# Kernel tuning notes

Hardware: AMD Instinct MI355X
Metric: run time of the kernel (lower is better)

## Reference

```python
import jax, jax.numpy as jnp
import numpy as np
from jax import lax

# Static config (matches init_kwargs)
D_MODEL = 1024
EXPAND = 2
D_INNER = D_MODEL * EXPAND          # 2048
HEAD_DIM = 64
N_HEADS = D_INNER // HEAD_DIM       # 32
N_GROUPS = 1
D_STATE = 128
D_CONV = 4
CONV_DIM = D_INNER + 2 * N_GROUPS * D_STATE        # 2304
D_IN_PROJ = 2 * D_INNER + 2 * N_GROUPS * D_STATE + N_HEADS  # 4384
SEQLEN = 8192
LN_EPS = 1e-5


def setup_inputs() -> dict:
    key = jax.random.key(0)
    ks = jax.random.split(key, 6)
    x = jax.random.normal(ks[0], (SEQLEN, D_MODEL), jnp.float32)
    W_in = jax.random.normal(ks[1], (D_IN_PROJ, D_MODEL), jnp.float32) / np.sqrt(D_MODEL)
    W_conv = jax.random.normal(ks[2], (CONV_DIM, 1, D_CONV), jnp.float32) / np.sqrt(D_CONV)
    b_conv = jnp.zeros((CONV_DIM,), jnp.float32)
    # dt_bias init per Mamba2: dt ~ LogUniform(dt_min, dt_max), inverse-softplus
    dt = jnp.exp(jax.random.uniform(ks[3], (N_HEADS,)) * (np.log(0.1) - np.log(0.001)) + np.log(0.001))
    dt = jnp.clip(dt, 1e-4)
    dt_bias = dt + jnp.log(-jnp.expm1(-dt))
    A_log = jnp.log(jax.random.uniform(ks[4], (N_HEADS,), minval=1.0, maxval=16.0))
    D_param = jnp.ones((N_HEADS,), jnp.float32)
    ln_w = jnp.ones((D_INNER,), jnp.float32)
    ln_b = jnp.zeros((D_INNER,), jnp.float32)
    W_out = jax.random.normal(ks[5], (D_MODEL, D_INNER), jnp.float32) / np.sqrt(D_INNER)
    return dict(x=x, W_in=W_in, W_conv=W_conv, b_conv=b_conv, dt_bias=dt_bias,
                A_log=A_log, D_param=D_param, ln_w=ln_w, ln_b=ln_b, W_out=W_out)


def reference(x, W_in, W_conv, b_conv, dt_bias, A_log, D_param, ln_w, ln_b, W_out):
    L = x.shape[0]
    zxbcdt = x @ W_in.T                                   # (L, d_in_proj)
    z = zxbcdt[:, :D_INNER]                               # gate
    xbc = zxbcdt[:, D_INNER:D_INNER + CONV_DIM]           # (L, conv_dim)
    dt = jax.nn.softplus(zxbcdt[:, D_INNER + CONV_DIM:] + dt_bias)  # (L, h)
    # depthwise causal-window conv with SAME padding over the sequence
    lhs = xbc.T[None]                                      # (1, conv_dim, L)
    conv = lax.conv_general_dilated(lhs, W_conv, (1,), 'SAME',
                                    feature_group_count=CONV_DIM,
                                    dimension_numbers=('NCH', 'OIH', 'NCH'))[0]
    xbc = jax.nn.silu((conv + b_conv[:, None]).T)          # (L, conv_dim)
    x_ssm = xbc[:, :D_INNER].reshape(L, N_HEADS, HEAD_DIM)
    B = xbc[:, D_INNER:D_INNER + N_GROUPS * D_STATE].reshape(L, N_GROUPS, D_STATE)
    C = xbc[:, D_INNER + N_GROUPS * D_STATE:].reshape(L, N_GROUPS, D_STATE)
    hpg = N_HEADS // N_GROUPS
    Bh = jnp.repeat(B, hpg, axis=1)                        # (L, h, n)
    Ch = jnp.repeat(C, hpg, axis=1)                        # (L, h, n)
    A = -jnp.exp(A_log)                                    # (h,), negative
    a = jnp.exp(dt * A)                                    # (L, h) per-token decay in (0,1)
    V = x_ssm * dt[..., None]                              # discretized input (L, h, p)
    # non-causal SSD (VSSD): global state H then readout, plus D skip
    H = jnp.einsum('lhn,lh,lhp->hnp', Bh, a, V)            # (h, n, p)
    y = jnp.einsum('lhn,hnp->lhp', Ch, H) + D_param[None, :, None] * x_ssm
    y = y.reshape(L, D_INNER)
    # LayerNorm (eqx default: weight+bias, eps=1e-5), then gate by z
    mu = jnp.mean(y, axis=-1, keepdims=True)
    var = jnp.var(y, axis=-1, keepdims=True)
    y = ((y - mu) / jnp.sqrt(var + LN_EPS)) * ln_w + ln_b
    y = y * z
    return y @ W_out.T                                     # (L, d_model)
```

## Files before the change

kernel.cpp:

```cpp
#include <hip/hip_runtime.h>
#include <hip/hip_bf16.h>
#include <math.h>

#define L_SEQ 8192
#define DM 1024
#define DI 2048
#define NH 32
#define HD 64
#define DS 128
#define CDIM 2304
#define DPROJ 4384
#define NPAD_IN 4608
#define KSPLIT 16
#define OPROWS 2176

typedef short bf16x8 __attribute__((ext_vector_type(8)));
typedef float floatx4 __attribute__((ext_vector_type(4)));
typedef unsigned short u16x4 __attribute__((ext_vector_type(4)));
typedef unsigned short u16x8 __attribute__((ext_vector_type(8)));

#define AS1(p) ((const __attribute__((address_space(1))) void*)(p))
#define AS3(p) ((__attribute__((address_space(3))) void*)(p))

__device__ __forceinline__ float bf2f(unsigned short u) {
  union { unsigned int i; float f; } c; c.i = ((unsigned int)u) << 16; return c.f;
}
__device__ __forceinline__ unsigned short f2bf(float f) {
  return __bfloat16_as_ushort(__float2bfloat16(f));
}

template <int OMODE>
__global__ __launch_bounds__(512, 6)
void gemm128_tlp3(const unsigned short* __restrict__ A, int lda,
                  const unsigned short* __restrict__ B, int ldb,
                  void* __restrict__ Cout, int ldc,
                  int K, int Nstore) {
  __shared__ __align__(16) char lds[49152];
  const int t = threadIdx.x;
  const int lane = t & 63;
  const int w = t >> 6;
  const int wm = w & 1, wn = w >> 1;
  const int fr = lane & 15, quad = lane >> 4;

  int gx = gridDim.x, gy = gridDim.y;
  int linear = blockIdx.y * gx + blockIdx.x;
  int xcd = linear & 7, loc = linear >> 3;
  int mper = gy >> 3;
  int mt = xcd * mper + loc % mper;
  int nt = loc / mper;
  const int m0 = mt << 7, n0 = nt << 7;
  const int NT = K >> 5;

  floatx4 acc[4][2];
#pragma unroll
  for (int i = 0; i < 4; ++i)
#pragma unroll
    for (int j = 0; j < 2; ++j) acc[i][j] = (floatx4){0.f, 0.f, 0.f, 0.f};
  bf16x8 af[4], bb[2];

  auto stA = [&](int slot, int kt) {
    int o = t * 16;
    int os = o ^ (((o >> 7) & 7) << 4);
    int r128 = os >> 7, half = (os >> 6) & 1, kb = os & 63;
    int R = (half << 6) | r128;
    const unsigned short* src = A + (size_t)(m0 + R) * lda + (kt << 5) + (kb >> 1);
    __builtin_amdgcn_global_load_lds(AS1(src), AS3(lds + slot * 16384 + o), 16, 0, 0);
  };
  auto stB = [&](int slot, int kt) {
    int o = t * 16;
    int os = o ^ (((o >> 7) & 7) << 4);
    int r128 = os >> 7, half = (os >> 6) & 1, kb = os & 63;
    int R = (half << 6) | r128;
    const unsigned short* src = B + (size_t)(n0 + R) * ldb + (kt << 5) + (kb >> 1);
    __builtin_amdgcn_global_load_lds(AS1(src), AS3(lds + slot * 16384 + 8192 + o), 16, 0, 0);
  };
  auto rdA = [&](int slot, int mi) -> bf16x8 {
    int r128 = (mi << 4) | fr;
    int chunk = ((wm << 2) | quad) ^ (fr & 7);
    return *(const bf16x8*)(lds + slot * 16384 + r128 * 128 + chunk * 16);
  };
  auto rdB = [&](int slot, int ni) -> bf16x8 {
    int R = (wn << 5) | (ni << 4) | fr;
    int r128 = R & 63, half = R >> 6;
    int chunk = ((half << 2) | quad) ^ (fr & 7);
    return *(const bf16x8*)(lds + slot * 16384 + 8192 + r128 * 128 + chunk * 16);
  };

  stA(0, 0); stB(0, 0);
  if (NT > 1) {
    stA(1, 1); stB(1, 1);
    asm volatile("s_waitcnt vmcnt(2)" ::: "memory");
  } else {
    asm volatile("s_waitcnt vmcnt(0)" ::: "memory");
  }
  __builtin_amdgcn_s_barrier();

  int cur = 0;
  for (int kt = 0; kt < NT; ++kt) {
    const bool pf = (kt + 2 < NT);
#pragma unroll
    for (int mi = 0; mi < 4; ++mi) af[mi] = rdA(cur, mi);
    bb[0] = rdB(cur, 0); bb[1] = rdB(cur, 1);
    if (pf) {
      int s2 = cur + 2; if (s2 >= 3) s2 -= 3;
      stA(s2, kt + 2); stB(s2, kt + 2);
    }
    asm volatile("s_waitcnt lgkmcnt(0)" ::: "memory");
    __builtin_amdgcn_s_setprio(1);
#pragma unroll
    for (int mi = 0; mi < 4; ++mi) {
      acc[mi][0] = __builtin_amdgcn_mfma_f32_16x16x32_bf16(af[mi], bb[0], acc[mi][0], 0, 0, 0);
      acc[mi][1] = __builtin_amdgcn_mfma_f32_16x16x32_bf16(af[mi], bb[1], acc[mi][1], 0, 0, 0);
    }
    __builtin_amdgcn_s_setprio(0);
    if (kt < NT - 1) {
      if (pf) asm volatile("s_waitcnt vmcnt(2)" ::: "memory");
      else    asm volatile("s_waitcnt vmcnt(0)" ::: "memory");
      __builtin_amdgcn_s_barrier();
    }
    ++cur; if (cur == 3) cur = 0;
  }

  if (OMODE == 0) {
    __syncthreads();
    unsigned short* rp = (unsigned short*)lds;
    unsigned short* C = (unsigned short*)Cout;
    const int mb = wm * 64, nb = wn * 32;
#pragma unroll
    for (int mi = 0; mi < 4; ++mi)
#pragma unroll
      for (int ni = 0; ni < 2; ++ni)
#pragma unroll
        for (int r = 0; r < 4; ++r)
          rp[(mb + mi * 16 + quad * 4 + r) * 128 + nb + ni * 16 + fr] = f2bf(acc[mi][ni][r]);
    __syncthreads();
#pragma unroll
    for (int j = 0; j < 4; ++j) {
      int lin = j * 4096 + t * 8;
      int row = lin >> 7, col = lin & 127;
      int gcol = n0 + col;
      if (gcol < Nstore)
        *(u16x8*)&C[(size_t)(m0 + row) * ldc + gcol] = *(const u16x8*)&rp[lin];
    }
  } else {
    float* Cf = (float*)Cout;
#pragma unroll
    for (int mi = 0; mi < 4; ++mi)
#pragma unroll
      for (int ni = 0; ni < 2; ++ni) {
        int gcol = n0 + wn * 32 + ni * 16 + fr;
        int grow = m0 + wm * 64 + mi * 16 + quad * 4;
#pragma unroll
        for (int r = 0; r < 4; ++r)
          if (gcol < Nstore)
            Cf[(size_t)(grow + r) * ldc + gcol] = acc[mi][ni][r];
      }
  }
}

template <int MODE>
__global__ __launch_bounds__(256)
void gemm_bt_mfma(const unsigned short* __restrict__ A, int lda,
                  const unsigned short* __restrict__ B, int ldb,
                  void* __restrict__ Cout, int ldc,
                  int Kfull, int Nstore,
                  const unsigned short* __restrict__ xs,
                  const float* __restrict__ Dvec) {
  __shared__ __align__(16) char smem[17408];
  unsigned short* Asm = (unsigned short*)smem;
  unsigned short* Bsm = Asm + 128 * 32;
  const int t = threadIdx.x;

  int bx = blockIdx.x, by = blockIdx.y;
  if (MODE != 2) {
    int gx = gridDim.x;
    int linear = by * gx + bx;
    int xcd = linear & 7;
    int local = linear >> 3;
    by = xcd * 8 + (local & 7);
    bx = local >> 3;
  }
  const int m0 = by * 128;
  const int n0 = bx * 128;

  int kstart = 0, klen = Kfull;
  if (MODE == 2) { klen = Kfull / KSPLIT; kstart = blockIdx.z * klen; }
  const int wave = t >> 6, lane = t & 63;
  const int wm = (wave & 1) * 64;
  const int wn = (wave >> 1) * 64;
  const int fr = lane & 15;
  const int quad = lane >> 4;

  floatx4 acc[4][4];
#pragma unroll
  for (int i = 0; i < 4; ++i)
#pragma unroll
    for (int j = 0; j < 4; ++j) acc[i][j] = (floatx4){0.f, 0.f, 0.f, 0.f};

  for (int k0 = kstart; k0 < kstart + klen; k0 += 32) {
#pragma unroll
    for (int i = 0; i < 2; ++i) {
      int linear = i * 256 + t;
      int row = linear >> 2;
      int kq = (linear & 3) * 8;
      const unsigned short* ga = A + (size_t)(m0 + row) * lda + (k0 + kq);
      const unsigned short* gb = B + (size_t)(n0 + row) * ldb + (k0 + kq);
      __builtin_amdgcn_global_load_lds(AS1(ga), AS3(&Asm[linear * 8]), 16, 0, 0);
      __builtin_amdgcn_global_load_lds(AS1(gb), AS3(&Bsm[linear * 8]), 16, 0, 0);
    }
    __syncthreads();

    bf16x8 af[4], bfr[4];
#pragma unroll
    for (int i = 0; i < 4; ++i) {
      af[i]  = *(const bf16x8*)&Asm[(wm + i * 16 + fr) * 32 + quad * 8];
      bfr[i] = *(const bf16x8*)&Bsm[(wn + i * 16 + fr) * 32 + quad * 8];
    }
#pragma unroll
    for (int mi = 0; mi < 4; ++mi)
#pragma unroll
      for (int ni = 0; ni < 4; ++ni)
        acc[mi][ni] = __builtin_amdgcn_mfma_f32_16x16x32_bf16(
            af[mi], bfr[ni], acc[mi][ni], 0, 0, 0);
    __syncthreads();
  }

  const int lrbase = (wm ? 16 : 0) + quad * 4;
  if (MODE == 0 || MODE == 1) {
    unsigned short(*rp)[136] = (unsigned short(*)[136])smem;
    unsigned short* C = (unsigned short*)Cout;
#pragma unroll
    for (int mi = 0; mi < 4; ++mi) {
      __syncthreads();
#pragma unroll
      for (int ni = 0; ni < 4; ++ni)
#pragma unroll
        for (int r = 0; r < 4; ++r)
          rp[lrbase + r][wn + ni * 16 + fr] = f2bf(acc[mi][ni][r]);
      __syncthreads();
#pragma unroll
      for (int j = 0; j < 2; ++j) {
        int off = j * 2048 + t * 8;
        int lr = off >> 7, c = off & 127;
        int grow = m0 + (lr >> 4) * 64 + mi * 16 + (lr & 15);
        int gcol = n0 + c;
        u16x8 v = *(const u16x8*)&rp[lr][c];
        if (MODE == 1) {
          u16x8 xv = *(const u16x8*)&xs[(size_t)grow * ldc + gcol];
          float Dh = Dvec[gcol >> 6];
          u16x8 o;
#pragma unroll
          for (int e = 0; e < 8; ++e) o[e] = f2bf(bf2f(v[e]) + Dh * bf2f(xv[e]));
          *(u16x8*)&C[(size_t)grow * ldc + gcol] = o;
        } else {
          if (gcol < Nstore) *(u16x8*)&C[(size_t)grow * ldc + gcol] = v;
        }
      }
    }
  } else {
    float(*rpf)[136] = (float(*)[136])smem;
    float* C = (float*)Cout;
    if (MODE == 2) C += (size_t)blockIdx.z * DS * DI;
#pragma unroll
    for (int mi = 0; mi < 4; ++mi) {
      __syncthreads();
#pragma unroll
      for (int ni = 0; ni < 4; ++ni)
#pragma unroll
        for (int r = 0; r < 4; ++r)
          rpf[lrbase + r][wn + ni * 16 + fr] = acc[mi][ni][r];
      __syncthreads();
#pragma unroll
      for (int j = 0; j < 4; ++j) {
        int off = j * 1024 + t * 4;
        int lr = off >> 7, c = off & 127;
        int grow = m0 + (lr >> 4) * 64 + mi * 16 + (lr & 15);
        int gcol = n0 + c;
        float4 v = *(const float4*)&rpf[lr][c];
        *(float4*)&C[(size_t)grow * ldc + gcol] = v;
      }
    }
  }
}

__global__ __launch_bounds__(256)
void cast_all_kernel(const float* __restrict__ x, const float* __restrict__ W_in,
                     const float* __restrict__ W_out,
                     unsigned short* __restrict__ x_bf16,
                     unsigned short* __restrict__ win_bf16,
                     unsigned short* __restrict__ wout_bf16) {
  int b = blockIdx.x;
  int t = threadIdx.x;
  u16x4 o = (u16x4){0, 0, 0, 0};
  if (b < 8192) {
    size_t i4 = ((size_t)b * 256 + t) * 4;
    float4 v = *(const float4*)(x + i4);
    o.x = f2bf(v.x); o.y = f2bf(v.y); o.z = f2bf(v.z); o.w = f2bf(v.w);
    *(u16x4*)(x_bf16 + i4) = o;
  } else if (b < 12800) {
    size_t i4 = ((size_t)(b - 8192) * 256 + t) * 4;
    int row = (int)(i4 >> 10);
    if (row < DPROJ) {
      float4 v = *(const float4*)(W_in + i4);
      o.x = f2bf(v.x); o.y = f2bf(v.y); o.z = f2bf(v.z); o.w = f2bf(v.w);
    }
    *(u16x4*)(win_bf16 + i4) = o;
  } else {
    size_t i4 = ((size_t)(b - 12800) * 256 + t) * 4;
    float4 v = *(const float4*)(W_out + i4);
    o.x = f2bf(v.x); o.y = f2bf(v.y); o.z = f2bf(v.z); o.w = f2bf(v.w);
    *(u16x4*)(wout_bf16 + i4) = o;
  }
}

__global__ __launch_bounds__(256)
void dt_kernel(const unsigned short* __restrict__ zxb, const float* __restrict__ dt_bias,
               const float* __restrict__ A_log, float* __restrict__ s_out) {
  int idx = blockIdx.x * 256 + threadIdx.x;
  int l = idx >> 5, h = idx & 31;
  float v = bf2f(zxb[(size_t)l * DPROJ + (DI + CDIM) + h]) + dt_bias[h];
  float d = (v > 20.f) ? v : log1pf(expf(v));
  s_out[idx] = d * expf(-d * expf(A_log[h]));
}

__global__ __launch_bounds__(256)
void conv_fused_kernel(const unsigned short* __restrict__ zxb,
                       const float* __restrict__ Wc,
                       const float* __restrict__ bc,
                       const float* __restrict__ svec,
                       unsigned short* __restrict__ xs,
                       unsigned short* __restrict__ cb,
                       unsigned short* __restrict__ OpT) {
  __shared__ unsigned short zt[67][66];
  __shared__ unsigned short ot[64][66];
  __shared__ float sl[64];
  const int c0 = blockIdx.x * 64;
  const int l0 = blockIdx.y * 64;
  const int t = threadIdx.x;
  for (int idx = t; idx < 67 * 16; idx += 256) {
    int row = idx >> 4;
    int colq = (idx & 15) * 4;
    int gl = l0 - 1 + row;
    u16x4 v = (u16x4){0, 0, 0, 0};
    if (gl >= 0 && gl < L_SEQ)
      v = *(const u16x4*)&zxb[(size_t)gl * DPROJ + DI + c0 + colq];
    *(u16x4*)&zt[row][colq] = v;
  }
  const bool isX = (c0 < DI);
  const bool isC = (c0 >= DI + DS);
  if (isX && t < 64) sl[t] = svec[(size_t)(l0 + t) * NH + (c0 >> 6)];
  const int c = t & 63;
  const int gc = c0 + c;
  const float4 wv = *(const float4*)&Wc[gc * 4];
  const float bias = bc[gc];
  const int lq = (t >> 6) * 16;
  __syncthreads();
#pragma unroll
  for (int i = 0; i < 16; ++i) {
    int ll = lq + i;
    float sacc = bias + bf2f(zt[ll][c]) * wv.x + bf2f(zt[ll + 1][c]) * wv.y +
                 bf2f(zt[ll + 2][c]) * wv.z + bf2f(zt[ll + 3][c]) * wv.w;
    float v = sacc / (1.f + expf(-sacc));
    int gl = l0 + ll;
    if (isC) {
      cb[(size_t)gl * DS + (gc - (DI + DS))] = f2bf(v);
    } else if (isX) {
      xs[(size_t)gl * DI + gc] = f2bf(v);
      ot[c][ll] = f2bf(v * sl[ll]);
    } else {
      ot[c][ll] = f2bf(v);
    }
  }
  if (!isC) {
    __syncthreads();
#pragma unroll
    for (int j = 0; j < 4; ++j) {
      int linear = j * 1024 + t * 4;
      int rr = linear >> 6;
      int lc = linear & 63;
      *(u16x4*)&OpT[(size_t)(c0 + rr) * L_SEQ + l0 + lc] = *(const u16x4*)&ot[rr][lc];
    }
  }
}

__global__ __launch_bounds__(256)
void h_reduce_t_kernel(const float* __restrict__ P, unsigned short* __restrict__ Ht) {
  __shared__ float tile[32][65];
  const int bid = blockIdx.x;
  const int pt = bid & 31, ng = bid >> 5;
  const int t = threadIdx.x;
#pragma unroll
  for (int i = 0; i < 8; ++i) {
    int nl = i * 4 + (t >> 6);
    int n = ng * 32 + nl;
    int p = pt * 64 + (t & 63);
    float acc = 0.f;
#pragma unroll
    for (int z = 0; z < KSPLIT; ++z)
      acc += P[(size_t)z * (DS * DI) + (size_t)n * DI + p];
    tile[nl][t & 63] = acc;
  }
  __syncthreads();
#pragma unroll
  for (int j = 0; j < 8; ++j) {
    int linear = j * 256 + t;
    int pl = linear >> 5, nl = linear & 31;
    Ht[(size_t)(pt * 64 + pl) * DS + ng * 32 + nl] = f2bf(tile[nl][pl]);
  }
}

__global__ __launch_bounds__(256)
void ln_mul_kernel(const unsigned short* __restrict__ ybuf, unsigned short* __restrict__ zxb,
                   const float* __restrict__ ln_w, const float* __restrict__ ln_b) {
  int l = blockIdx.x;
  int t = threadIdx.x;
  int c0 = t * 8;
  u16x8 yv = *(const u16x8*)&ybuf[(size_t)l * DI + c0];
  float vals[8];
  float s = 0.f, sq = 0.f;
#pragma unroll
  for (int i = 0; i < 8; ++i) {
    float v = bf2f(yv[i]);
    vals[i] = v;
    s += v;
    sq += v * v;
  }
#pragma unroll
  for (int off = 32; off > 0; off >>= 1) {
    s += __shfl_down(s, off, 64);
    sq += __shfl_down(sq, off, 64);
  }
  __shared__ float red[10];
  int wave = t >> 6, lane = t & 63;
  if (lane == 0) { red[wave] = s; red[4 + wave] = sq; }
  __syncthreads();
  if (t == 0) {
    float S = red[0] + red[1] + red[2] + red[3];
    float SQ = red[4] + red[5] + red[6] + red[7];
    float mu = S / (float)DI;
    red[8] = mu;
    red[9] = rsqrtf(SQ / (float)DI - mu * mu + 1e-5f);
  }
  __syncthreads();
  float mu = red[8], rstd = red[9];
  unsigned short* zrow = zxb + (size_t)l * DPROJ;
  u16x8 zv = *(const u16x8*)&zrow[c0];
  float4 w0 = *(const float4*)&ln_w[c0], w1 = *(const float4*)&ln_w[c0 + 4];
  float4 b0 = *(const float4*)&ln_b[c0], b1 = *(const float4*)&ln_b[c0 + 4];
  float w[8] = {w0.x, w0.y, w0.z, w0.w, w1.x, w1.y, w1.z, w1.w};
  float b[8] = {b0.x, b0.y, b0.z, b0.w, b1.x, b1.y, b1.z, b1.w};
  u16x8 o;
#pragma unroll
  for (int i = 0; i < 8; ++i) {
    float v = (vals[i] - mu) * rstd * w[i] + b[i];
    o[i] = f2bf(v * bf2f(zv[i]));
  }
  *(u16x8*)&zrow[DI + c0] = o;
}

extern "C" void kernel_launch(void* const* d_in, const int* in_sizes, int n_in,
                              void* d_out, int out_size, void* d_ws, size_t ws_size,
                              hipStream_t stream) {
  const float* x       = (const float*)d_in[0];
  const float* W_in    = (const float*)d_in[1];
  const float* W_conv  = (const float*)d_in[2];
  const float* b_conv  = (const float*)d_in[3];
  const float* dt_bias = (const float*)d_in[4];
  const float* A_log   = (const float*)d_in[5];
  const float* D_param = (const float*)d_in[6];
  const float* ln_w    = (const float*)d_in[7];
  const float* ln_b    = (const float*)d_in[8];
  const float* W_out   = (const float*)d_in[9];
  float* out = (float*)d_out;

  unsigned short* zxb = (unsigned short*)d_ws;
  unsigned short* xs   = zxb + (size_t)L_SEQ * DPROJ;
  unsigned short* cb   = xs + (size_t)L_SEQ * DI;
  float* svec = (float*)(cb + (size_t)L_SEQ * DS);
  unsigned short* OpT = (unsigned short*)(svec + (size_t)L_SEQ * NH);
  float* Ppart = (float*)(OpT + (size_t)OPROWS * L_SEQ);
  unsigned short* Ht = (unsigned short*)(Ppart + (size_t)KSPLIT * DS * DI);
  unsigned short* wout_bf16 = Ht + (size_t)DI * DS;
  unsigned short* x_bf16   = OpT;
  unsigned short* win_bf16 = OpT + (size_t)L_SEQ * DM;
  unsigned short* ybuf     = OpT;

  cast_all_kernel<<<14848, 256, 0, stream>>>(x, W_in, W_out, x_bf16, win_bf16,
                                             wout_bf16);

  gemm128_tlp3<0><<<dim3(NPAD_IN / 128, L_SEQ / 128), 512, 0, stream>>>(
      x_bf16, DM, win_bf16, DM, zxb, DPROJ, DM, DPROJ);

  dt_kernel<<<(L_SEQ * NH) / 256, 256, 0, stream>>>(zxb, dt_bias, A_log, svec);

  conv_fused_kernel<<<dim3(CDIM / 64, L_SEQ / 64), 256, 0, stream>>>(
      zxb, W_conv, b_conv, svec, xs, cb, OpT);

  gemm_bt_mfma<2><<<dim3(DI / 128, 1, KSPLIT), 256, 0, stream>>>(
      OpT + (size_t)DI * L_SEQ, L_SEQ, OpT, L_SEQ, Ppart, DI, L_SEQ, DI,
      nullptr, nullptr);

  h_reduce_t_kernel<<<128, 256, 0, stream>>>(Ppart, Ht);

  gemm_bt_mfma<1><<<dim3(DI / 128, L_SEQ / 128), 256, 0, stream>>>(
      cb, DS, Ht, DS, ybuf, DI, DS, DI, xs, D_param);

  ln_mul_kernel<<<L_SEQ, 256, 0, stream>>>(ybuf, zxb, ln_w, ln_b);

  gemm128_tlp3<1><<<dim3(DM / 128, L_SEQ / 128), 512, 0, stream>>>(
      zxb + DI, DPROJ, wout_bf16, DI, out, DM, DI, DM);
}
```

Baseline: 340.1 us.

## Enlarge GEMM block tile to 256x128 with 4x2 warp layout

Changes the bf16 MFMA GEMM used for the input and output projections from a 128x128 to a 256x128 block tile. Each warp now computes a 64x64 sub-tile with 16 accumulators, and the B fragments are reloaded in two halves. The aim is more MFMA work per LDS load and less global traffic per output, at the cost of more LDS (72KB), more registers, lower occupancy (launch bound 4) and half as many blocks. The epilogue LDS staging now writes 256 rows x 128 bf16, which is 64KB and still fits in the 72KB buffer.

New measurement: 328.9 us. -3.3%, faster.

```diff
diff --git a/kernel.cpp b/kernel.cpp
--- a/kernel.cpp
+++ b/kernel.cpp
@@ -30,16 +30,16 @@
 }
 
 template <int OMODE>
-__global__ __launch_bounds__(512, 6)
-void gemm128_tlp3(const unsigned short* __restrict__ A, int lda,
-                  const unsigned short* __restrict__ B, int ldb,
-                  void* __restrict__ Cout, int ldc,
-                  int K, int Nstore) {
-  __shared__ __align__(16) char lds[49152];
+__global__ __launch_bounds__(512, 4)
+void gemm_v4(const unsigned short* __restrict__ A, int lda,
+             const unsigned short* __restrict__ B, int ldb,
+             void* __restrict__ Cout, int ldc,
+             int K, int Nstore) {
+  __shared__ __align__(16) char lds[73728];
   const int t = threadIdx.x;
   const int lane = t & 63;
   const int w = t >> 6;
-  const int wm = w & 1, wn = w >> 1;
+  const int wm = w & 3, wn = w >> 2;
   const int fr = lane & 15, quad = lane >> 4;
 
   int gx = gridDim.x, gy = gridDim.y;
@@ -48,48 +48,56 @@
   int mper = gy >> 3;
   int mt = xcd * mper + loc % mper;
   int nt = loc / mper;
-  const int m0 = mt << 7, n0 = nt << 7;
+  const int m0 = mt << 8, n0 = nt << 7;
   const int NT = K >> 5;
 
-  floatx4 acc[4][2];
+  floatx4 acc[4][4];
 #pragma unroll
   for (int i = 0; i < 4; ++i)
 #pragma unroll
-    for (int j = 0; j < 2; ++j) acc[i][j] = (floatx4){0.f, 0.f, 0.f, 0.f};
+    for (int j = 0; j < 4; ++j) acc[i][j] = (floatx4){0.f, 0.f, 0.f, 0.f};
   bf16x8 af[4], bb[2];
 
   auto stA = [&](int slot, int kt) {
-    int o = t * 16;
-    int os = o ^ (((o >> 7) & 7) << 4);
-    int r128 = os >> 7, half = (os >> 6) & 1, kb = os & 63;
-    int R = (half << 6) | r128;
-    const unsigned short* src = A + (size_t)(m0 + R) * lda + (kt << 5) + (kb >> 1);
-    __builtin_amdgcn_global_load_lds(AS1(src), AS3(lds + slot * 16384 + o), 16, 0, 0);
+#pragma unroll
+    for (int i = 0; i < 2; ++i) {
+      int o = i * 8192 + t * 16;
+      int os = o ^ (((o >> 7) & 7) << 4);
+      int r128 = os >> 7;
+      int half = (os >> 6) & 1;
+      int kb = os & 63;
+      int R = (half << 7) | r128;
+      const unsigned short* src = A + (size_t)(m0 + R) * lda + (kt << 5) + (kb >> 1);
+      __builtin_amdgcn_global_load_lds(AS1(src), AS3(lds + slot * 24576 + o), 16, 0, 0);
+    }
   };
   auto stB = [&](int slot, int kt) {
     int o = t * 16;
     int os = o ^ (((o >> 7) & 7) << 4);
-    int r128 = os >> 7, half = (os >> 6) & 1, kb = os & 63;
-    int R = (half << 6) | r128;
+    int r64 = os >> 7;
+    int half = (os >> 6) & 1;
+    int kb = os & 63;
+    int R = (half << 6) | r64;
     const unsigned short* src = B + (size_t)(n0 + R) * ldb + (kt << 5) + (kb >> 1);
-    __builtin_amdgcn_global_load_lds(AS1(src), AS3(lds + slot * 16384 + 8192 + o), 16, 0, 0);
+    __builtin_amdgcn_global_load_lds(AS1(src), AS3(lds + slot * 24576 + 16384 + o), 16, 0, 0);
   };
   auto rdA = [&](int slot, int mi) -> bf16x8 {
-    int r128 = (mi << 4) | fr;
-    int chunk = ((wm << 2) | quad) ^ (fr & 7);
-    return *(const bf16x8*)(lds + slot * 16384 + r128 * 128 + chunk * 16);
+    int R = (wm << 6) | (mi << 4) | fr;
+    int r128 = R & 127, half = R >> 7;
+    int chunk = ((half << 2) | quad) ^ (fr & 7);
+    return *(const bf16x8*)(lds + slot * 24576 + r128 * 128 + chunk * 16);
   };
   auto rdB = [&](int slot, int ni) -> bf16x8 {
-    int R = (wn << 5) | (ni << 4) | fr;
-    int r128 = R & 63, half = R >> 6;
+    int R = (wn << 6) | (ni << 4) | fr;
+    int r64 = R & 63, half = R >> 6;
     int chunk = ((half << 2) | quad) ^ (fr & 7);
-    return *(const bf16x8*)(lds + slot * 16384 + 8192 + r128 * 128 + chunk * 16);
+    return *(const bf16x8*)(lds + slot * 24576 + 16384 + r64 * 128 + chunk * 16);
   };
 
   stA(0, 0); stB(0, 0);
   if (NT > 1) {
     stA(1, 1); stB(1, 1);
-    asm volatile("s_waitcnt vmcnt(2)" ::: "memory");
+    asm volatile("s_waitcnt vmcnt(3)" ::: "memory");
   } else {
     asm volatile("s_waitcnt vmcnt(0)" ::: "memory");
   }
@@ -113,8 +121,17 @@
       acc[mi][1] = __builtin_amdgcn_mfma_f32_16x16x32_bf16(af[mi], bb[1], acc[mi][1], 0, 0, 0);
     }
     __builtin_amdgcn_s_setprio(0);
+    bb[0] = rdB(cur, 2); bb[1] = rdB(cur, 3);
+    asm volatile("s_waitcnt lgkmcnt(0)" ::: "memory");
+    __builtin_amdgcn_s_setprio(1);
+#pragma unroll
+    for (int mi = 0; mi < 4; ++mi) {
+      acc[mi][2] = __builtin_amdgcn_mfma_f32_16x16x32_bf16(af[mi], bb[0], acc[mi][2], 0, 0, 0);
+      acc[mi][3] = __builtin_amdgcn_mfma_f32_16x16x32_bf16(af[mi], bb[1], acc[mi][3], 0, 0, 0);
+    }
+    __builtin_amdgcn_s_setprio(0);
     if (kt < NT - 1) {
-      if (pf) asm volatile("s_waitcnt vmcnt(2)" ::: "memory");
+      if (pf) asm volatile("s_waitcnt vmcnt(3)" ::: "memory");
       else    asm volatile("s_waitcnt vmcnt(0)" ::: "memory");
       __builtin_amdgcn_s_barrier();
     }
@@ -125,17 +142,17 @@
     __syncthreads();
     unsigned short* rp = (unsigned short*)lds;
     unsigned short* C = (unsigned short*)Cout;
-    const int mb = wm * 64, nb = wn * 32;
+    const int mb = wm * 64, nb = wn * 64;
 #pragma unroll
     for (int mi = 0; mi < 4; ++mi)
 #pragma unroll
-      for (int ni = 0; ni < 2; ++ni)
+      for (int ni = 0; ni < 4; ++ni)
 #pragma unroll
         for (int r = 0; r < 4; ++r)
           rp[(mb + mi * 16 + quad * 4 + r) * 128 + nb + ni * 16 + fr] = f2bf(acc[mi][ni][r]);
     __syncthreads();
 #pragma unroll
-    for (int j = 0; j < 4; ++j) {
+    for (int j = 0; j < 8; ++j) {
       int lin = j * 4096 + t * 8;
       int row = lin >> 7, col = lin & 127;
       int gcol = n0 + col;
@@ -147,8 +164,8 @@
 #pragma unroll
     for (int mi = 0; mi < 4; ++mi)
 #pragma unroll
-      for (int ni = 0; ni < 2; ++ni) {
-        int gcol = n0 + wn * 32 + ni * 16 + fr;
+      for (int ni = 0; ni < 4; ++ni) {
+        int gcol = n0 + wn * 64 + ni * 16 + fr;
         int grow = m0 + wm * 64 + mi * 16 + quad * 4;
 #pragma unroll
         for (int r = 0; r < 4; ++r)
@@ -488,7 +505,7 @@
   cast_all_kernel<<<14848, 256, 0, stream>>>(x, W_in, W_out, x_bf16, win_bf16,
                                              wout_bf16);
 
-  gemm128_tlp3<0><<<dim3(NPAD_IN / 128, L_SEQ / 128), 512, 0, stream>>>(
+  gemm_v4<0><<<dim3(NPAD_IN / 128, L_SEQ / 256), 512, 0, stream>>>(
       x_bf16, DM, win_bf16, DM, zxb, DPROJ, DM, DPROJ);
 
   dt_kernel<<<(L_SEQ * NH) / 256, 256, 0, stream>>>(zxb, dt_bias, A_log, svec);
@@ -507,6 +524,6 @@
 
   ln_mul_kernel<<<L_SEQ, 256, 0, stream>>>(ybuf, zxb, ln_w, ln_b);
 
-  gemm128_tlp3<1><<<dim3(DM / 128, L_SEQ / 128), 512, 0, stream>>>(
+  gemm_v4<1><<<dim3(DM / 128, L_SEQ / 256), 512, 0, stream>>>(
       zxb + DI, DPROJ, wout_bf16, DI, out, DM, DI, DM);
 }
```
